# Optimization experiments

Measured on AMD Instinct MI355X. Metric: run time of the kernel, lower is better.

Reference implementation:

```python
import jax, jax.numpy as jnp
import numpy as np

C = 128
EPS = 1e-5


def _ln(x, g, b):
    m = jnp.mean(x, axis=-1, keepdims=True)
    v = jnp.mean((x - m) ** 2, axis=-1, keepdims=True)
    return (x - m) * jax.lax.rsqrt(v + EPS) * g + b


def setup_inputs() -> dict:
    key = jax.random.key(0)
    ks = jax.random.split(key, 10)
    B, N = 1, 384
    s = 1.0 / np.sqrt(C)
    inp = {
        "z": jax.random.normal(ks[0], (B, N, N, C), dtype=jnp.float32),
        "ln1_g": jnp.ones((C,), jnp.float32),
        "ln1_b": jnp.zeros((C,), jnp.float32),
        "ln2_g": jnp.ones((C,), jnp.float32),
        "ln2_b": jnp.zeros((C,), jnp.float32),
        "Wa": jax.random.uniform(ks[1], (C, C), jnp.float32, -s, s),
        "ba": jnp.zeros((C,), jnp.float32),
        "Wga": jax.random.uniform(ks[2], (C, C), jnp.float32, -s, s),
        "bga": jnp.zeros((C,), jnp.float32),
        "Wb": jax.random.uniform(ks[3], (C, C), jnp.float32, -s, s),
        "bb": jnp.zeros((C,), jnp.float32),
        "Wgb": jax.random.uniform(ks[4], (C, C), jnp.float32, -s, s),
        "bgb": jnp.zeros((C,), jnp.float32),
        "Wg": jax.random.uniform(ks[5], (C, C), jnp.float32, -s, s),
        "bg": jnp.zeros((C,), jnp.float32),
        "Wo": jax.random.uniform(ks[6], (C, C), jnp.float32, -s, s),
        "bo": jnp.zeros((C,), jnp.float32),
    }
    return inp


def reference(z, ln1_g, ln1_b, ln2_g, ln2_b, Wa, ba, Wga, bga, Wb, bb, Wgb, bgb, Wg, bg, Wo, bo):
    # z: (B, i, j, c)
    zn = _ln(z, ln1_g, ln1_b)
    a = (zn @ Wa + ba) * jax.nn.sigmoid(zn @ Wga + bga)      # (B,i,k,c)
    b = (zn @ Wb + bb) * jax.nn.sigmoid(zn @ Wgb + bgb)      # (B,j,k,c)
    gate = jax.nn.sigmoid(zn @ Wg + bg)                      # (B,i,j,c)
    o = jnp.einsum('bikc,bjkc->bijc', a, b)                  # outgoing triangle update
    return gate * (_ln(o, ln2_g, ln2_b) @ Wo + bo)
```

## Files before the change

### kernel.cpp

```cpp
#include <hip/hip_runtime.h>
#include <stdint.h>

typedef _Float16 f16x8 __attribute__((ext_vector_type(8)));
typedef float floatx4 __attribute__((ext_vector_type(4)));
typedef unsigned int u32x4 __attribute__((ext_vector_type(4)));

#define RR 147456
#define NC 128
#define NN 384

__device__ inline floatx4 zero4() { floatx4 v; v[0]=0.f; v[1]=0.f; v[2]=0.f; v[3]=0.f; return v; }
__device__ inline float sigmoidf_(float x) { return 1.f / (1.f + __expf(-x)); }

__global__ __launch_bounds__(256) void k0_wt(
    const float* __restrict__ w0, const float* __restrict__ w1,
    const float* __restrict__ w2, const float* __restrict__ w3,
    const float* __restrict__ w4, const float* __restrict__ w5,
    _Float16* __restrict__ wf)
{
  const float* w;
  switch (blockIdx.x) {
    case 0: w = w0; break; case 1: w = w1; break; case 2: w = w2; break;
    case 3: w = w3; break; case 4: w = w4; break; default: w = w5; break;
  }
  _Float16* out = wf + blockIdx.x * 16384;
  const int t = threadIdx.x;
  for (int it = 0; it < 64; ++it) {
    int f = it * 256 + t;
    int j  = f & 7;
    int ln = (f >> 3) & 63;
    int nt = (f >> 9) & 7;
    int k0 = f >> 12;
    int k = k0 * 32 + (ln >> 4) * 8 + j;
    int n = nt * 16 + (ln & 15);
    out[f] = (_Float16)w[k * 128 + n];
  }
}

__global__ __launch_bounds__(256, 3) void k2_ln_gemm(
    const float* __restrict__ z, const float* __restrict__ ln1g, const float* __restrict__ ln1b,
    const _Float16* __restrict__ wf,
    const float* __restrict__ ba, const float* __restrict__ bga,
    const float* __restrict__ bb, const float* __restrict__ bgb,
    const float* __restrict__ bg,
    _Float16* __restrict__ at, _Float16* __restrict__ bt, _Float16* __restrict__ gate)
{
  __shared__ __align__(16) _Float16 zns[64][136];
  __shared__ __align__(16) _Float16 bnc[4][32 * 72];
  const int t = threadIdx.x;
  const int w = t >> 6, lane = t & 63;
  const int l15 = lane & 15, quad = lane >> 4;
  const int r0 = blockIdx.x * 64;
  const int nt0 = w * 2;

  {
    const int g = lane >> 4, h = lane & 15;
    float4 ga = *(const float4*)(ln1g + h*8);
    float4 gb = *(const float4*)(ln1g + h*8 + 4);
    float4 bba = *(const float4*)(ln1b + h*8);
    float4 bbb = *(const float4*)(ln1b + h*8 + 4);
    #pragma unroll
    for (int rr = 0; rr < 4; ++rr) {
      int row = w * 16 + rr * 4 + g;
      const float* zp = z + (size_t)(r0 + row) * NC + h * 8;
      float4 xa = *(const float4*)zp;
      float4 xb = *(const float4*)(zp + 4);
      float s = xa.x + xa.y + xa.z + xa.w + xb.x + xb.y + xb.z + xb.w;
      float q = xa.x*xa.x + xa.y*xa.y + xa.z*xa.z + xa.w*xa.w
              + xb.x*xb.x + xb.y*xb.y + xb.z*xb.z + xb.w*xb.w;
      #pragma unroll
      for (int m = 1; m < 16; m <<= 1) { s += __shfl_xor(s, m); q += __shfl_xor(q, m); }
      float mean = s * (1.f/128.f);
      float var  = q * (1.f/128.f) - mean*mean;
      float rs = rsqrtf(var + 1e-5f);
      union { uint4 u; _Float16 hh[8]; } pk;
      pk.hh[0] = (_Float16)((xa.x - mean) * rs * ga.x + bba.x);
      pk.hh[1] = (_Float16)((xa.y - mean) * rs * ga.y + bba.y);
      pk.hh[2] = (_Float16)((xa.z - mean) * rs * ga.z + bba.z);
      pk.hh[3] = (_Float16)((xa.w - mean) * rs * ga.w + bba.w);
      pk.hh[4] = (_Float16)((xb.x - mean) * rs * gb.x + bbb.x);
      pk.hh[5] = (_Float16)((xb.y - mean) * rs * gb.y + bbb.y);
      pk.hh[6] = (_Float16)((xb.z - mean) * rs * gb.z + bbb.z);
      pk.hh[7] = (_Float16)((xb.w - mean) * rs * gb.w + bbb.w);
      *(uint4*)&zns[row][h * 8] = pk.u;
    }
  }
  __syncthreads();

  const _Float16* pw = wf + lane * 8;
  f16x8 bwA[4][2], bwB[4][2];
  floatx4 acc[4][2];
  union PkU { unsigned int u; _Float16 h[2]; };
  PkU sig[4][2][2];

  auto loadw = [&](f16x8 (&bw)[4][2], int slot) {
    const _Float16* p = pw + slot * 16384;
    #pragma unroll
    for (int k0 = 0; k0 < 4; ++k0)
      #pragma unroll
      for (int j = 0; j < 2; ++j)
        bw[k0][j] = *(const f16x8*)(p + (k0*8 + nt0 + j) * 512);
  };
  auto dogemm = [&](const f16x8 (&bw)[4][2]) {
    #pragma unroll
    for (int mt = 0; mt < 4; ++mt) {
      acc[mt][0] = zero4(); acc[mt][1] = zero4();
      #pragma unroll
      for (int k0 = 0; k0 < 4; ++k0) {
        f16x8 af = *(const f16x8*)&zns[mt*16 + l15][k0*32 + quad*8];
        acc[mt][0] = __builtin_amdgcn_mfma_f32_16x16x32_f16(af, bw[k0][0], acc[mt][0], 0, 0, 0);
        acc[mt][1] = __builtin_amdgcn_mfma_f32_16x16x32_f16(af, bw[k0][1], acc[mt][1], 0, 0, 0);
      }
    }
  };
  auto sigpack = [&](const float* big) {
    #pragma unroll
    for (int j = 0; j < 2; ++j) {
      float bgv = big[(nt0 + j)*16 + l15];
      #pragma unroll
      for (int mt = 0; mt < 4; ++mt) {
        sig[mt][j][0].h[0] = (_Float16)sigmoidf_(acc[mt][j][0] + bgv);
        sig[mt][j][0].h[1] = (_Float16)sigmoidf_(acc[mt][j][1] + bgv);
        sig[mt][j][1].h[0] = (_Float16)sigmoidf_(acc[mt][j][2] + bgv);
        sig[mt][j][1].h[1] = (_Float16)sigmoidf_(acc[mt][j][3] + bgv);
      }
    }
  };
  auto bounce_out = [&](_Float16* dst) {
    asm volatile("s_waitcnt lgkmcnt(0)" ::: "memory");
    _Float16* base = dst + (size_t)blockIdx.x * 8192 + w * 2048;
    #pragma unroll
    for (int i = 0; i < 4; ++i) {
      int f = i * 512 + lane * 8;
      int cp = f >> 6, pos = f & 63;
      u32x4 v = *(const u32x4*)&bnc[w][cp * 72 + pos];
      *(u32x4*)(base + f) = v;
    }
  };
  auto combine_store = [&](const float* bia, _Float16* dst) {
    #pragma unroll
    for (int j = 0; j < 2; ++j) {
      int c = (nt0 + j)*16 + l15;
      float bav = bia[c];
      #pragma unroll
      for (int mt = 0; mt < 4; ++mt) {
        union { uint2 u2; _Float16 h[4]; } pk;
        pk.h[0] = (_Float16)((acc[mt][j][0] + bav) * (float)sig[mt][j][0].h[0]);
        pk.h[1] = (_Float16)((acc[mt][j][1] + bav) * (float)sig[mt][j][0].h[1]);
        pk.h[2] = (_Float16)((acc[mt][j][2] + bav) * (float)sig[mt][j][1].h[0]);
        pk.h[3] = (_Float16)((acc[mt][j][3] + bav) * (float)sig[mt][j][1].h[1]);
        *(uint2*)&bnc[w][(j*16 + l15) * 72 + mt*16 + quad*4] = pk.u2;
      }
    }
    bounce_out(dst);
  };

  loadw(bwA, 1); loadw(bwB, 0);
  dogemm(bwA); sigpack(bga);
  loadw(bwA, 3);
  dogemm(bwB); combine_store(ba, at);
  loadw(bwB, 2);
  dogemm(bwA); sigpack(bgb);
  loadw(bwA, 4);
  dogemm(bwB); combine_store(bb, bt);
  dogemm(bwA);
  #pragma unroll
  for (int j = 0; j < 2; ++j) {
    float bgv = bg[(nt0 + j)*16 + l15];
    #pragma unroll
    for (int mt = 0; mt < 4; ++mt) {
      union { uint2 u2; _Float16 h[4]; } pk;
      #pragma unroll
      for (int r = 0; r < 4; ++r)
        pk.h[r] = (_Float16)sigmoidf_(acc[mt][j][r] + bgv);
      *(uint2*)&bnc[w][(j*16 + l15) * 72 + mt*16 + quad*4] = pk.u2;
    }
  }
  bounce_out(gate);
}

__global__ __launch_bounds__(256, 3) void k3_tri(
    const _Float16* __restrict__ at, const _Float16* __restrict__ bt, _Float16* __restrict__ o)
{
  __shared__ __align__(16) _Float16 As[2][128 * 40];
  __shared__ __align__(16) _Float16 Bs[2][128 * 40];
  const int t = threadIdx.x;
  const int w = t >> 6, lane = t & 63, l15 = lane & 15, quad = lane >> 4;
  const int c = blockIdx.y;
  const int i0 = (blockIdx.x / 3) * 128, j0 = (blockIdx.x % 3) * 128;
  const int wi = w >> 1, wj = w & 1;

  const int srow = t >> 1, sch = (t & 1) * 16;
  const _Float16* gaRow = at + (size_t)(i0 + srow) * 6 * 8192 + (size_t)c * 64;
  const _Float16* gbRow = bt + (size_t)(j0 + srow) * 6 * 8192 + (size_t)c * 64;
  _Float16* const pa0 = &As[0][srow * 40 + sch];
  _Float16* const pb0 = &Bs[0][srow * 40 + sch];
  _Float16* const pa1 = &As[1][srow * 40 + sch];
  _Float16* const pb1 = &Bs[1][srow * 40 + sch];

  floatx4 acc[4][4];
  #pragma unroll
  for (int mt = 0; mt < 4; ++mt)
    #pragma unroll
    for (int nt = 0; nt < 4; ++nt) acc[mt][nt] = zero4();

  f16x8 aP0,aP1,bP0,bP1, aQ0,aQ1,bQ0,bQ1;

  auto gofs = [&](int kk) -> size_t {
    int x = kk + sch;
    return (size_t)(x >> 6) * 8192 + (size_t)(x & 63);
  };
  auto gloadP = [&](int kk) {
    size_t go = gofs(kk);
    aP0 = *(const f16x8*)(gaRow + go); aP1 = *(const f16x8*)(gaRow + go + 8);
    bP0 = *(const f16x8*)(gbRow + go); bP1 = *(const f16x8*)(gbRow + go + 8);
  };
  auto gloadQ = [&](int kk) {
    size_t go = gofs(kk);
    aQ0 = *(const f16x8*)(gaRow + go); aQ1 = *(const f16x8*)(gaRow + go + 8);
    bQ0 = *(const f16x8*)(gbRow + go); bQ1 = *(const f16x8*)(gbRow + go + 8);
  };
  auto swriteP = [&](int buf) {
    _Float16* pa = buf ? pa1 : pa0; _Float16* pb = buf ? pb1 : pb0;
    *(f16x8*)pa = aP0; *(f16x8*)(pa + 8) = aP1;
    *(f16x8*)pb = bP0; *(f16x8*)(pb + 8) = bP1;
  };
  auto swriteQ = [&](int buf) {
    _Float16* pa = buf ? pa1 : pa0; _Float16* pb = buf ? pb1 : pb0;
    *(f16x8*)pa = aQ0; *(f16x8*)(pa + 8) = aQ1;
    *(f16x8*)pb = bQ0; *(f16x8*)(pb + 8) = bQ1;
  };
  auto compute = [&](int buf) {
    f16x8 af[4], bfr[4];
    #pragma unroll
    for (int mt = 0; mt < 4; ++mt)
      af[mt] = *(const f16x8*)&As[buf][(wi*64 + mt*16 + l15) * 40 + quad*8];
    #pragma unroll
    for (int nt = 0; nt < 4; ++nt)
      bfr[nt] = *(const f16x8*)&Bs[buf][(wj*64 + nt*16 + l15) * 40 + quad*8];
    #pragma unroll
    for (int mt = 0; mt < 4; ++mt)
      #pragma unroll
      for (int nt = 0; nt < 4; ++nt)
        acc[mt][nt] = __builtin_amdgcn_mfma_f32_16x16x32_f16(af[mt], bfr[nt], acc[mt][nt], 0, 0, 0);
  };

  gloadP(0); swriteP(0); gloadP(32);
  __syncthreads();
  #pragma unroll
  for (int s = 0; s < 12; s += 2) {
    if (s + 2 < 12) gloadQ((s + 2) * 32);
    compute(0);
    swriteP(1);
    __syncthreads();
    if (s + 3 < 12) gloadP((s + 3) * 32);
    compute(1);
    if (s + 2 < 12) { swriteQ(0); __syncthreads(); }
  }

  #pragma unroll
  for (int mt = 0; mt < 4; ++mt) {
    #pragma unroll
    for (int r = 0; r < 4; ++r) {
      int i = i0 + wi*64 + mt*16 + quad*4 + r;
      _Float16* obase = o + (size_t)(i*6 + (j0 >> 6) + wj) * 8192 + (size_t)c * 64;
      #pragma unroll
      for (int nt = 0; nt < 4; ++nt)
        obase[nt*16 + l15] = (_Float16)acc[mt][nt][r];
    }
  }
}

__global__ __launch_bounds__(256, 4) void k4_out(
    const _Float16* __restrict__ o, const _Float16* __restrict__ gate,
    const float* __restrict__ ln2g, const float* __restrict__ ln2b,
    const _Float16* __restrict__ wo5, const float* __restrict__ bo,
    float* __restrict__ out)
{
  __shared__ __align__(16) _Float16 osb[64][136];
  const int t = threadIdx.x;
  const int w = t >> 6, lane = t & 63, l15 = lane & 15, quad = lane >> 4;
  const int r0 = blockIdx.x * 64;
  const int nt0 = w * 2;

  f16x8 bw[4][2];
  {
    const _Float16* p = wo5 + lane * 8;
    #pragma unroll
    for (int k0 = 0; k0 < 4; ++k0)
      #pragma unroll
      for (int j = 0; j < 2; ++j)
        bw[k0][j] = *(const f16x8*)(p + (k0*8 + nt0 + j) * 512);
  }
  union GkU { uint2 u2; _Float16 h[4]; };
  GkU gk[2][4];
  #pragma unroll
  for (int j = 0; j < 2; ++j) {
    int cch = (nt0 + j)*16 + l15;
    #pragma unroll
    for (int mt = 0; mt < 4; ++mt)
      gk[j][mt].u2 = *(const uint2*)(gate + (size_t)blockIdx.x * 8192 + (size_t)cch * 64 + mt*16 + quad*4);
  }

  {
    const _Float16* ob = o + (size_t)blockIdx.x * 8192;
    #pragma unroll
    for (int it = 0; it < 4; ++it) {
      int f = (it * 256 + t) * 8;
      int cx = f >> 6, p = f & 63;
      f16x8 v = *(const f16x8*)(ob + f);
      #pragma unroll
      for (int i = 0; i < 8; ++i) osb[p + i][cx] = v[i];
    }
  }
  __syncthreads();

  {
    const int g = lane >> 4, h = lane & 15;
    float4 ga = *(const float4*)(ln2g + h*8);
    float4 gb = *(const float4*)(ln2g + h*8 + 4);
    float4 bba = *(const float4*)(ln2b + h*8);
    float4 bbb = *(const float4*)(ln2b + h*8 + 4);
    #pragma unroll
    for (int rr = 0; rr < 4; ++rr) {
      int row = w * 16 + rr * 4 + g;
      f16x8 xv = *(const f16x8*)&osb[row][h*8];
      float x0 = (float)xv[0], x1 = (float)xv[1], x2 = (float)xv[2], x3 = (float)xv[3];
      float x4 = (float)xv[4], x5 = (float)xv[5], x6 = (float)xv[6], x7 = (float)xv[7];
      float s = x0+x1+x2+x3+x4+x5+x6+x7;
      float q = x0*x0+x1*x1+x2*x2+x3*x3+x4*x4+x5*x5+x6*x6+x7*x7;
      #pragma unroll
      for (int m = 1; m < 16; m <<= 1) { s += __shfl_xor(s, m); q += __shfl_xor(q, m); }
      float mean = s * (1.f/128.f);
      float var  = q * (1.f/128.f) - mean*mean;
      float rs = rsqrtf(var + 1e-5f);
      union { uint4 u; _Float16 hh[8]; } pk;
      pk.hh[0] = (_Float16)((x0 - mean) * rs * ga.x + bba.x);
      pk.hh[1] = (_Float16)((x1 - mean) * rs * ga.y + bba.y);
      pk.hh[2] = (_Float16)((x2 - mean) * rs * ga.z + bba.z);
      pk.hh[3] = (_Float16)((x3 - mean) * rs * ga.w + bba.w);
      pk.hh[4] = (_Float16)((x4 - mean) * rs * gb.x + bbb.x);
      pk.hh[5] = (_Float16)((x5 - mean) * rs * gb.y + bbb.y);
      pk.hh[6] = (_Float16)((x6 - mean) * rs * gb.z + bbb.z);
      pk.hh[7] = (_Float16)((x7 - mean) * rs * gb.w + bbb.w);
      *(uint4*)&osb[row][h * 8] = pk.u;
    }
  }
  __syncthreads();

  floatx4 acc[4][2];
  #pragma unroll
  for (int mt = 0; mt < 4; ++mt) {
    acc[mt][0] = zero4(); acc[mt][1] = zero4();
    #pragma unroll
    for (int k0 = 0; k0 < 4; ++k0) {
      f16x8 af = *(const f16x8*)&osb[mt*16 + l15][k0*32 + quad*8];
      acc[mt][0] = __builtin_amdgcn_mfma_f32_16x16x32_f16(af, bw[k0][0], acc[mt][0], 0, 0, 0);
      acc[mt][1] = __builtin_amdgcn_mfma_f32_16x16x32_f16(af, bw[k0][1], acc[mt][1], 0, 0, 0);
    }
  }

  #pragma unroll
  for (int j = 0; j < 2; ++j) {
    int cch = (nt0 + j)*16 + l15;
    float bov = bo[cch];
    #pragma unroll
    for (int mt = 0; mt < 4; ++mt) {
      #pragma unroll
      for (int r = 0; r < 4; ++r) {
        int rl = mt*16 + quad*4 + r;
        __builtin_nontemporal_store((float)gk[j][mt].h[r] * (acc[mt][j][r] + bov),
                                    out + (size_t)(r0 + rl) * NC + cch);
      }
    }
  }
}

extern "C" void kernel_launch(void* const* d_in, const int* in_sizes, int n_in,
                              void* d_out, int out_size, void* d_ws, size_t ws_size,
                              hipStream_t stream) {
  const float* z    = (const float*)d_in[0];
  const float* l1g  = (const float*)d_in[1];
  const float* l1b  = (const float*)d_in[2];
  const float* l2g  = (const float*)d_in[3];
  const float* l2b  = (const float*)d_in[4];
  const float* Wa   = (const float*)d_in[5];
  const float* ba   = (const float*)d_in[6];
  const float* Wga  = (const float*)d_in[7];
  const float* bga  = (const float*)d_in[8];
  const float* Wb   = (const float*)d_in[9];
  const float* bb   = (const float*)d_in[10];
  const float* Wgb  = (const float*)d_in[11];
  const float* bgb  = (const float*)d_in[12];
  const float* Wg   = (const float*)d_in[13];
  const float* bg   = (const float*)d_in[14];
  const float* Wo   = (const float*)d_in[15];
  const float* bo   = (const float*)d_in[16];

  char* ws = (char*)d_ws;
  _Float16* at_  = (_Float16*)(ws + 0);
  _Float16* bt_  = (_Float16*)(ws + 37748736);
  _Float16* gate = (_Float16*)(ws + 75497472);
  _Float16* o16  = (_Float16*)(ws + 113246208);
  _Float16* wf   = (_Float16*)(ws + 188743680);

  hipLaunchKernelGGL(k0_wt, dim3(6), dim3(256), 0, stream, Wa, Wga, Wb, Wgb, Wg, Wo, wf);
  hipLaunchKernelGGL(k2_ln_gemm, dim3(2304), dim3(256), 0, stream,
                     z, l1g, l1b, wf, ba, bga, bb, bgb, bg, at_, bt_, gate);
  hipLaunchKernelGGL(k3_tri, dim3(9, 128), dim3(256), 0, stream, at_, bt_, o16);
  hipLaunchKernelGGL(k4_out, dim3(2304), dim3(256), 0, stream,
                     o16, gate, l2g, l2b, wf + 5*16384, bo, (float*)d_out);
}
```

Baseline: 280.1 us.

## Deepen einsum register prefetch to three stages and swizzle k4 LDS tile

The triangle-einsum kernel now keeps three register staging sets instead of two. Global loads are issued two k-steps ahead of the shared-memory writes, which hides more memory latency behind the MFMA compute, and the loop is fully unrolled. Separately, the output kernel's transposed LDS tile uses an XOR swizzle on 8-element column groups so the scattered transpose writes and the later vector reads conflict less on LDS banks. The cost is more live registers in the einsum kernel, which may reduce occupancy.

```diff
diff --git a/kernel.cpp b/kernel.cpp
--- a/kernel.cpp
+++ b/kernel.cpp
@@ -204,31 +204,43 @@
     #pragma unroll
     for (int nt = 0; nt < 4; ++nt) acc[mt][nt] = zero4();
 
-  f16x8 aP0,aP1,bP0,bP1, aQ0,aQ1,bQ0,bQ1;
+  f16x8 a00,a01,b00,b01;
+  f16x8 a10,a11,b10,b11;
+  f16x8 a20,a21,b20,b21;
 
   auto gofs = [&](int kk) -> size_t {
     int x = kk + sch;
     return (size_t)(x >> 6) * 8192 + (size_t)(x & 63);
   };
-  auto gloadP = [&](int kk) {
+  auto gload0 = [&](int kk) {
     size_t go = gofs(kk);
-    aP0 = *(const f16x8*)(gaRow + go); aP1 = *(const f16x8*)(gaRow + go + 8);
-    bP0 = *(const f16x8*)(gbRow + go); bP1 = *(const f16x8*)(gbRow + go + 8);
-  };
-  auto gloadQ = [&](int kk) {
+    a00 = *(const f16x8*)(gaRow + go); a01 = *(const f16x8*)(gaRow + go + 8);
+    b00 = *(const f16x8*)(gbRow + go); b01 = *(const f16x8*)(gbRow + go + 8);
+  };
+  auto gload1 = [&](int kk) {
     size_t go = gofs(kk);
-    aQ0 = *(const f16x8*)(gaRow + go); aQ1 = *(const f16x8*)(gaRow + go + 8);
-    bQ0 = *(const f16x8*)(gbRow + go); bQ1 = *(const f16x8*)(gbRow + go + 8);
-  };
-  auto swriteP = [&](int buf) {
+    a10 = *(const f16x8*)(gaRow + go); a11 = *(const f16x8*)(gaRow + go + 8);
+    b10 = *(const f16x8*)(gbRow + go); b11 = *(const f16x8*)(gbRow + go + 8);
+  };
+  auto gload2 = [&](int kk) {
+    size_t go = gofs(kk);
+    a20 = *(const f16x8*)(gaRow + go); a21 = *(const f16x8*)(gaRow + go + 8);
+    b20 = *(const f16x8*)(gbRow + go); b21 = *(const f16x8*)(gbRow + go + 8);
+  };
+  auto swrite0 = [&](int buf) {
     _Float16* pa = buf ? pa1 : pa0; _Float16* pb = buf ? pb1 : pb0;
-    *(f16x8*)pa = aP0; *(f16x8*)(pa + 8) = aP1;
-    *(f16x8*)pb = bP0; *(f16x8*)(pb + 8) = bP1;
-  };
-  auto swriteQ = [&](int buf) {
+    *(f16x8*)pa = a00; *(f16x8*)(pa + 8) = a01;
+    *(f16x8*)pb = b00; *(f16x8*)(pb + 8) = b01;
+  };
+  auto swrite1 = [&](int buf) {
     _Float16* pa = buf ? pa1 : pa0; _Float16* pb = buf ? pb1 : pb0;
-    *(f16x8*)pa = aQ0; *(f16x8*)(pa + 8) = aQ1;
-    *(f16x8*)pb = bQ0; *(f16x8*)(pb + 8) = bQ1;
+    *(f16x8*)pa = a10; *(f16x8*)(pa + 8) = a11;
+    *(f16x8*)pb = b10; *(f16x8*)(pb + 8) = b11;
+  };
+  auto swrite2 = [&](int buf) {
+    _Float16* pa = buf ? pa1 : pa0; _Float16* pb = buf ? pb1 : pb0;
+    *(f16x8*)pa = a20; *(f16x8*)(pa + 8) = a21;
+    *(f16x8*)pb = b20; *(f16x8*)(pb + 8) = b21;
   };
   auto compute = [&](int buf) {
     f16x8 af[4], bfr[4];
@@ -245,18 +257,22 @@
         acc[mt][nt] = __builtin_amdgcn_mfma_f32_16x16x32_f16(af[mt], bfr[nt], acc[mt][nt], 0, 0, 0);
   };
 
-  gloadP(0); swriteP(0); gloadP(32);
+  gload0(0); gload1(32); gload2(64);
+  swrite0(0); swrite1(1);
+  gload0(96); gload1(128);
   __syncthreads();
-  #pragma unroll
-  for (int s = 0; s < 12; s += 2) {
-    if (s + 2 < 12) gloadQ((s + 2) * 32);
-    compute(0);
-    swriteP(1);
-    __syncthreads();
-    if (s + 3 < 12) gloadP((s + 3) * 32);
-    compute(1);
-    if (s + 2 < 12) { swriteQ(0); __syncthreads(); }
-  }
+  compute(0); __syncthreads(); swrite2(0); gload2(160);
+  compute(1); __syncthreads(); swrite0(1); gload0(192);
+  compute(0); __syncthreads(); swrite1(0); gload1(224);
+  compute(1); __syncthreads(); swrite2(1); gload2(256);
+  compute(0); __syncthreads(); swrite0(0); gload0(288);
+  compute(1); __syncthreads(); swrite1(1); gload1(320);
+  compute(0); __syncthreads(); swrite2(0); gload2(352);
+  compute(1); __syncthreads(); swrite0(1);
+  compute(0); __syncthreads(); swrite1(0);
+  compute(1); __syncthreads(); swrite2(1);
+  compute(0); __syncthreads();
+  compute(1);
 
   #pragma unroll
   for (int mt = 0; mt < 4; ++mt) {
@@ -309,8 +325,11 @@
       int f = (it * 256 + t) * 8;
       int cx = f >> 6, p = f & 63;
       f16x8 v = *(const f16x8*)(ob + f);
-      #pragma unroll
-      for (int i = 0; i < 8; ++i) osb[p + i][cx] = v[i];
+      int cxg = cx >> 3, cl = cx & 7;
+      int rg = p >> 3;
+      int col = ((cxg ^ rg) << 3) | cl;
+      #pragma unroll
+      for (int i = 0; i < 8; ++i) osb[p + i][col] = v[i];
     }
   }
   __syncthreads();
@@ -324,7 +343,8 @@
     #pragma unroll
     for (int rr = 0; rr < 4; ++rr) {
       int row = w * 16 + rr * 4 + g;
-      f16x8 xv = *(const f16x8*)&osb[row][h*8];
+      int col = ((h ^ (row >> 3)) << 3);
+      f16x8 xv = *(const f16x8*)&osb[row][col];
       float x0 = (float)xv[0], x1 = (float)xv[1], x2 = (float)xv[2], x3 = (float)xv[3];
       float x4 = (float)xv[4], x5 = (float)xv[5], x6 = (float)xv[6], x7 = (float)xv[7];
       float s = x0+x1+x2+x3+x4+x5+x6+x7;
@@ -343,7 +363,7 @@
       pk.hh[5] = (_Float16)((x5 - mean) * rs * gb.y + bbb.y);
       pk.hh[6] = (_Float16)((x6 - mean) * rs * gb.z + bbb.z);
       pk.hh[7] = (_Float16)((x7 - mean) * rs * gb.w + bbb.w);
-      *(uint4*)&osb[row][h * 8] = pk.u;
+      *(uint4*)&osb[row][col] = pk.u;
     }
   }
   __syncthreads();
@@ -354,7 +374,9 @@
     acc[mt][0] = zero4(); acc[mt][1] = zero4();
     #pragma unroll
     for (int k0 = 0; k0 < 4; ++k0) {
-      f16x8 af = *(const f16x8*)&osb[mt*16 + l15][k0*32 + quad*8];
+      int row = mt*16 + l15;
+      int col = (((k0*4 + quad) ^ (row >> 3)) << 3);
+      f16x8 af = *(const f16x8*)&osb[row][col];
       acc[mt][0] = __builtin_amdgcn_mfma_f32_16x16x32_f16(af, bw[k0][0], acc[mt][0], 0, 0, 0);
       acc[mt][1] = __builtin_amdgcn_mfma_f32_16x16x32_f16(af, bw[k0][1], acc[mt][1], 0, 0, 0);
     }
```

Measured after the change: 274.8 us. About the same (-1.9%).
